# Optimization experiments

Hardware: AMD Instinct MI355X
Metric: run time of the kernel (lower is better)

The kernel has to match this reference:

```python
import jax, jax.numpy as jnp
import numpy as np

N = 100000          # nodes
DEG = 16            # fixed in-degree -> E = N*DEG edges
E = N * DEG
NEG_SLOPE = 0.2
HEADS = 4
HID = 64            # per-head hidden dim; layer width = HEADS*HID = 256
IN_DIM = 256
NUM_CLASSES = 41


def setup_inputs() -> dict:
    key = jax.random.key(0)
    ks = jax.random.split(key, 12)
    # CSC-style structure: for destination node i, col_ind[row_ptr[i]:row_ptr[i+1]] are its source neighbors
    row_ptr = (jnp.arange(N + 1, dtype=jnp.int32) * DEG)
    col_ind = jax.random.randint(ks[0], (E,), 0, N, dtype=jnp.int32)
    inputs = jax.random.normal(ks[1], (N, IN_DIM), dtype=jnp.float32)

    def glorot(k, shape):
        fan = sum(shape)
        return jax.random.normal(k, shape, dtype=jnp.float32) * jnp.sqrt(2.0 / fan)

    W0 = glorot(ks[2], (IN_DIM, HEADS * HID))
    al0 = glorot(ks[3], (HEADS, HID)); ar0 = glorot(ks[4], (HEADS, HID))
    W1 = glorot(ks[5], (HEADS * HID, HEADS * HID))
    al1 = glorot(ks[6], (HEADS, HID)); ar1 = glorot(ks[7], (HEADS, HID))
    W2 = glorot(ks[8], (HEADS * HID, HEADS * NUM_CLASSES))
    al2 = glorot(ks[9], (HEADS, NUM_CLASSES)); ar2 = glorot(ks[10], (HEADS, NUM_CLASSES))
    return {"row_ptr": row_ptr, "col_ind": col_ind, "inputs": inputs,
            "W0": W0, "al0": al0, "ar0": ar0,
            "W1": W1, "al1": al1, "ar1": ar1,
            "W2": W2, "al2": al2, "ar2": ar2}


def _gat_conv(h, W, a_l, a_r, src, dst, out_dim):
    # h: [N, F_in] -> feat: [N, H, D]
    feat = (h @ W).reshape(N, HEADS, out_dim)
    el = jnp.einsum('nhd,hd->nh', feat, a_l)   # [N, H] source-side score
    er = jnp.einsum('nhd,hd->nh', feat, a_r)   # [N, H] dest-side score
    e = jax.nn.leaky_relu(el[src] + er[dst], NEG_SLOPE)  # [E, H]
    # edge softmax over incoming edges of each destination node
    emax = jax.ops.segment_max(e, dst, num_segments=N)
    ex = jnp.exp(e - emax[dst])
    denom = jax.ops.segment_sum(ex, dst, num_segments=N)
    alpha = ex / denom[dst]                     # [E, H]
    # attention-weighted aggregation of source features
    msg = alpha[:, :, None] * feat[src]         # [E, H, D]
    return jax.ops.segment_sum(msg, dst, num_segments=N)  # [N, H, D]


def reference(row_ptr, col_ind, inputs, W0, al0, ar0, W1, al1, ar1, W2, al2, ar2):
    deg = jnp.diff(row_ptr)
    dst = jnp.repeat(jnp.arange(N, dtype=jnp.int32), deg, total_repeat_length=E)
    src = col_ind
    h = _gat_conv(inputs, W0, al0, ar0, src, dst, HID).reshape(N, HEADS * HID)
    h = _gat_conv(h, W1, al1, ar1, src, dst, HID).reshape(N, HEADS * HID)
    logits = _gat_conv(h, W2, al2, ar2, src, dst, NUM_CLASSES).mean(axis=1)  # [N, C]
    return logits
```

## Files before the change

### kernel.cpp

```cpp
#include <hip/hip_runtime.h>

#define NN 100000
#define DEG 16
#define HEADS 4
#define NEG_SLOPE 0.2f
#define NPAD 100096

typedef unsigned short ushort_t;
typedef __attribute__((ext_vector_type(8))) short bf16x8;
typedef __attribute__((ext_vector_type(4))) float f32x4;

__device__ __forceinline__ ushort_t f2bf_rn(float f) {
    uint32_t u = __float_as_uint(f);
    uint32_t r = (u + 0x7fffu + ((u >> 16) & 1u)) >> 16;
    return (ushort_t)r;
}
__device__ __forceinline__ float bf2f(ushort_t u) {
    return __uint_as_float(((uint32_t)u) << 16);
}

__global__ __launch_bounds__(256) void prep_wt(
    const float* __restrict__ W, ushort_t* __restrict__ Wh,
    ushort_t* __restrict__ Wl, int ncr)
{
    int idx = blockIdx.x * 256 + threadIdx.x;
    int n = idx >> 8, k = idx & 255;
    float v = (n < ncr) ? W[k * ncr + n] : 0.f;
    uint32_t b  = __float_as_uint(v);
    uint32_t hb = b & 0xffff0000u;
    float r = v - __uint_as_float(hb);
    Wh[idx] = (ushort_t)(hb >> 16);
    Wl[idx] = (ushort_t)(__float_as_uint(r) >> 16);
}

template <int AMODE, bool DO_SCORES>
__global__ __launch_bounds__(256) void gemm_mfma(
    const float* __restrict__ A32,
    const ushort_t* __restrict__ Ahi, const ushort_t* __restrict__ Alo,
    const ushort_t* __restrict__ Bth, const ushort_t* __restrict__ Btl,
    const float* __restrict__ al, const float* __restrict__ ar,
    ushort_t* __restrict__ Cb, int ldc, int ncr,
    float* __restrict__ el, float* __restrict__ er)
{
    __shared__ uint4 smem[2048];

    const int tid  = threadIdx.x;
    const int wv   = tid >> 6;
    const int ln   = tid & 63;
    const int wm   = wv >> 1;
    const int wn   = wv & 1;
    const int cl   = ln & 15;
    const int kq   = ln >> 4;
    const int row0 = blockIdx.y * 128;
    const int col0 = blockIdx.x * 128;

    f32x4 acc[4][4] = {};

    for (int k0 = 0; k0 < 256; k0 += 64) {
        if (k0) __syncthreads();
        if (AMODE == 1) {
            #pragma unroll
            for (int p = 0; p < 4; ++p) {
                int s = p * 256 + tid;
                int row = s >> 3, c = s & 7;
                int csw = c ^ (row & 7);
                size_t g = (size_t)(row0 + row) * 256 + k0 + c * 8;
                smem[row * 8 + csw]        = *reinterpret_cast<const uint4*>(Ahi + g);
                smem[1024 + row * 8 + csw] = *reinterpret_cast<const uint4*>(Alo + g);
            }
        } else {
            #pragma unroll
            for (int p = 0; p < 4; ++p) {
                int s = p * 256 + tid;
                int row = s >> 3, c = s & 7;
                int csw = c ^ (row & 7);
                int gr = row0 + row;
                float4 v0 = make_float4(0.f,0.f,0.f,0.f), v1 = v0;
                if (gr < NN) {
                    const float* g = A32 + (size_t)gr * 256 + k0 + c * 8;
                    v0 = *reinterpret_cast<const float4*>(g);
                    v1 = *reinterpret_cast<const float4*>(g + 4);
                }
                uint32_t b0 = __float_as_uint(v0.x), b1 = __float_as_uint(v0.y);
                uint32_t b2 = __float_as_uint(v0.z), b3 = __float_as_uint(v0.w);
                uint32_t b4 = __float_as_uint(v1.x), b5 = __float_as_uint(v1.y);
                uint32_t b6 = __float_as_uint(v1.z), b7 = __float_as_uint(v1.w);
                uint4 vh;
                vh.x = (b1 & 0xffff0000u) | (b0 >> 16);
                vh.y = (b3 & 0xffff0000u) | (b2 >> 16);
                vh.z = (b5 & 0xffff0000u) | (b4 >> 16);
                vh.w = (b7 & 0xffff0000u) | (b6 >> 16);
                float r0 = v0.x - __uint_as_float(b0 & 0xffff0000u);
                float r1 = v0.y - __uint_as_float(b1 & 0xffff0000u);
                float r2 = v0.z - __uint_as_float(b2 & 0xffff0000u);
                float r3 = v0.w - __uint_as_float(b3 & 0xffff0000u);
                float r4 = v1.x - __uint_as_float(b4 & 0xffff0000u);
                float r5 = v1.y - __uint_as_float(b5 & 0xffff0000u);
                float r6 = v1.z - __uint_as_float(b6 & 0xffff0000u);
                float r7 = v1.w - __uint_as_float(b7 & 0xffff0000u);
                uint4 vl;
                vl.x = (__float_as_uint(r1) & 0xffff0000u) | (__float_as_uint(r0) >> 16);
                vl.y = (__float_as_uint(r3) & 0xffff0000u) | (__float_as_uint(r2) >> 16);
                vl.z = (__float_as_uint(r5) & 0xffff0000u) | (__float_as_uint(r4) >> 16);
                vl.w = (__float_as_uint(r7) & 0xffff0000u) | (__float_as_uint(r6) >> 16);
                smem[row * 8 + csw]        = vh;
                smem[1024 + row * 8 + csw] = vl;
            }
        }
        __syncthreads();

        #pragma unroll
        for (int ksub = 0; ksub < 2; ++ksub) {
            bf16x8 ah[4], ax[4];
            #pragma unroll
            for (int mf = 0; mf < 4; ++mf) {
                int row = wm * 64 + mf * 16 + cl;
                int chunk = (ksub * 4 + kq) ^ (row & 7);
                int idx = row * 8 + chunk;
                ah[mf] = ((const bf16x8*)smem)[idx];
                ax[mf] = ((const bf16x8*)smem)[1024 + idx];
            }
            #pragma unroll
            for (int nf = 0; nf < 4; ++nf) {
                int colg = col0 + wn * 64 + nf * 16 + cl;
                size_t boff = (size_t)colg * 256 + k0 + ksub * 32 + kq * 8;
                bf16x8 bh = *reinterpret_cast<const bf16x8*>(Bth + boff);
                bf16x8 bl = *reinterpret_cast<const bf16x8*>(Btl + boff);
                #pragma unroll
                for (int mf = 0; mf < 4; ++mf) {
                    acc[mf][nf] = __builtin_amdgcn_mfma_f32_16x16x32_bf16(ah[mf], bh, acc[mf][nf], 0, 0, 0);
                    acc[mf][nf] = __builtin_amdgcn_mfma_f32_16x16x32_bf16(ah[mf], bl, acc[mf][nf], 0, 0, 0);
                    acc[mf][nf] = __builtin_amdgcn_mfma_f32_16x16x32_bf16(ax[mf], bh, acc[mf][nf], 0, 0, 0);
                }
            }
        }
    }

    #pragma unroll
    for (int mf = 0; mf < 4; ++mf) {
        int gr0 = row0 + wm * 64 + mf * 16 + kq * 4;
        #pragma unroll
        for (int r = 0; r < 4; ++r) {
            int gr = gr0 + r;
            if (gr < NN) {
                #pragma unroll
                for (int nf = 0; nf < 4; ++nf) {
                    int gc = col0 + wn * 64 + nf * 16 + cl;
                    if (gc < ncr)
                        Cb[(size_t)gr * ldc + gc] = f2bf_rn(acc[mf][nf][r]);
                }
            }
        }
    }

    if (DO_SCORES) {
        const int head = blockIdx.x * 2 + wn;
        float alv[4], arv[4];
        #pragma unroll
        for (int nf = 0; nf < 4; ++nf) {
            int d = nf * 16 + cl;
            alv[nf] = al[head * 64 + d];
            arv[nf] = ar[head * 64 + d];
        }
        #pragma unroll
        for (int mf = 0; mf < 4; ++mf) {
            #pragma unroll
            for (int r = 0; r < 4; ++r) {
                float pl = 0.f, pr = 0.f;
                #pragma unroll
                for (int nf = 0; nf < 4; ++nf) {
                    pl += acc[mf][nf][r] * alv[nf];
                    pr += acc[mf][nf][r] * arv[nf];
                }
                #pragma unroll
                for (int msk = 1; msk <= 8; msk <<= 1) {
                    pl += __shfl_xor(pl, msk);
                    pr += __shfl_xor(pr, msk);
                }
                if (cl == 0) {
                    int gr = row0 + wm * 64 + mf * 16 + kq * 4 + r;
                    if (gr < NN) {
                        el[gr * HEADS + head] = pl;
                        er[gr * HEADS + head] = pr;
                    }
                }
            }
        }
    }
}

__global__ __launch_bounds__(256) void scores2_bf(
    const ushort_t* __restrict__ featb, const float* __restrict__ al,
    const float* __restrict__ ar, float* __restrict__ el, float* __restrict__ er)
{
    const int n = blockIdx.x;
    const int t = threadIdx.x;
    const int h = t >> 6;
    const int j = t & 63;
    float v = 0.f, u = 0.f;
    if (j < 41) {
        float f = bf2f(featb[(size_t)n * 164 + h * 41 + j]);
        v = f * al[h * 41 + j];
        u = f * ar[h * 41 + j];
    }
    #pragma unroll
    for (int off = 32; off > 0; off >>= 1) {
        v += __shfl_down(v, off);
        u += __shfl_down(u, off);
    }
    if (j == 0) {
        el[n * HEADS + h] = v;
        er[n * HEADS + h] = u;
    }
}

__global__ __launch_bounds__(256) void agg_full_bf(
    const ushort_t* __restrict__ featb, const float* __restrict__ el,
    const float* __restrict__ er, const int* __restrict__ col,
    ushort_t* __restrict__ Hhi, ushort_t* __restrict__ Hlo)
{
    __shared__ int   s_src[4][DEG];
    __shared__ float s_alpha[4][HEADS][DEG];

    const int t = threadIdx.x;
    const int w = t >> 6;
    const int l = t & 63;
    const int n = blockIdx.x * 4 + w;
    const int h = l >> 4;
    const int k = l & 15;

    const int src_k = col[n * DEG + k];
    float x = el[src_k * HEADS + h] + er[n * HEADS + h];
    x = x > 0.f ? x : NEG_SLOPE * x;

    float m = x;
    #pragma unroll
    for (int msk = 8; msk >= 1; msk >>= 1) m = fmaxf(m, __shfl_xor(m, msk));
    float ex = __expf(x - m);
    float s = ex;
    #pragma unroll
    for (int msk = 8; msk >= 1; msk >>= 1) s += __shfl_xor(s, msk);

    s_alpha[w][h][k] = ex / s;
    if (l < DEG) s_src[w][l] = src_k;
    __syncthreads();

    float4 acc = make_float4(0.f, 0.f, 0.f, 0.f);
    #pragma unroll
    for (int k2 = 0; k2 < DEG; ++k2) {
        const int   sk = s_src[w][k2];
        const float a  = s_alpha[w][h][k2];
        ushort4 f = *reinterpret_cast<const ushort4*>(&featb[(size_t)sk * 256 + l * 4]);
        acc.x += a * bf2f(f.x);
        acc.y += a * bf2f(f.y);
        acc.z += a * bf2f(f.z);
        acc.w += a * bf2f(f.w);
    }
    uint32_t bx = __float_as_uint(acc.x), by = __float_as_uint(acc.y);
    uint32_t bz = __float_as_uint(acc.z), bw = __float_as_uint(acc.w);
    ushort4 hv;
    hv.x = (ushort_t)(bx >> 16); hv.y = (ushort_t)(by >> 16);
    hv.z = (ushort_t)(bz >> 16); hv.w = (ushort_t)(bw >> 16);
    float rx = acc.x - __uint_as_float(bx & 0xffff0000u);
    float ry = acc.y - __uint_as_float(by & 0xffff0000u);
    float rz = acc.z - __uint_as_float(bz & 0xffff0000u);
    float rw = acc.w - __uint_as_float(bw & 0xffff0000u);
    ushort4 lv;
    lv.x = (ushort_t)(__float_as_uint(rx) >> 16);
    lv.y = (ushort_t)(__float_as_uint(ry) >> 16);
    lv.z = (ushort_t)(__float_as_uint(rz) >> 16);
    lv.w = (ushort_t)(__float_as_uint(rw) >> 16);
    *reinterpret_cast<ushort4*>(&Hhi[(size_t)n * 256 + l * 4]) = hv;
    *reinterpret_cast<ushort4*>(&Hlo[(size_t)n * 256 + l * 4]) = lv;
}

__global__ __launch_bounds__(256) void agg_out_bf(
    const ushort_t* __restrict__ featb, const float* __restrict__ el,
    const float* __restrict__ er, const int* __restrict__ col,
    float* __restrict__ out)
{
    __shared__ int   s_src[4][DEG];
    __shared__ float s_alpha[4][HEADS][DEG];
    __shared__ float s_agg[4][164];

    const int t = threadIdx.x;
    const int w = t >> 6;
    const int l = t & 63;
    const int n = blockIdx.x * 4 + w;
    const int h = l >> 4;
    const int k = l & 15;

    const int src_k = col[n * DEG + k];
    float x = el[src_k * HEADS + h] + er[n * HEADS + h];
    x = x > 0.f ? x : NEG_SLOPE * x;

    float m = x;
    #pragma unroll
    for (int msk = 8; msk >= 1; msk >>= 1) m = fmaxf(m, __shfl_xor(m, msk));
    float ex = __expf(x - m);
    float s = ex;
    #pragma unroll
    for (int msk = 8; msk >= 1; msk >>= 1) s += __shfl_xor(s, msk);

    s_alpha[w][h][k] = ex / s;
    if (l < DEG) s_src[w][l] = src_k;
    __syncthreads();

    const int l41 = l < 41 ? l : 40;
    const int c0 = 4 * l41;
    const int h0 = (c0 + 0) / 41, h1 = (c0 + 1) / 41;
    const int h2 = (c0 + 2) / 41, h3 = (c0 + 3) / 41;

    float4 acc = make_float4(0.f, 0.f, 0.f, 0.f);
    #pragma unroll
    for (int k2 = 0; k2 < DEG; ++k2) {
        const int sk = s_src[w][k2];
        ushort4 f = *reinterpret_cast<const ushort4*>(&featb[(size_t)sk * 164 + c0]);
        acc.x += s_alpha[w][h0][k2] * bf2f(f.x);
        acc.y += s_alpha[w][h1][k2] * bf2f(f.y);
        acc.z += s_alpha[w][h2][k2] * bf2f(f.z);
        acc.w += s_alpha[w][h3][k2] * bf2f(f.w);
    }
    if (l < 41) *reinterpret_cast<float4*>(&s_agg[w][c0]) = acc;
    __syncthreads();
    if (l < 41)
        out[(size_t)n * 41 + l] =
            0.25f * (s_agg[w][l] + s_agg[w][l + 41] + s_agg[w][l + 82] + s_agg[w][l + 123]);
}

extern "C" void kernel_launch(void* const* d_in, const int* in_sizes, int n_in,
                              void* d_out, int out_size, void* d_ws, size_t ws_size,
                              hipStream_t stream)
{
    const int*   col_ind = (const int*)  d_in[1];
    const float* inputs  = (const float*)d_in[2];
    const float* W0      = (const float*)d_in[3];
    const float* al0     = (const float*)d_in[4];
    const float* ar0     = (const float*)d_in[5];
    const float* W1      = (const float*)d_in[6];
    const float* al1     = (const float*)d_in[7];
    const float* ar1     = (const float*)d_in[8];
    const float* W2      = (const float*)d_in[9];
    const float* al2     = (const float*)d_in[10];
    const float* ar2     = (const float*)d_in[11];
    float* out = (float*)d_out;

    char* ws = (char*)d_ws;
    const size_t seg = (size_t)NPAD * 256 * sizeof(ushort_t);
    ushort_t* h_hi  = (ushort_t*)(ws);
    ushort_t* h_lo  = (ushort_t*)(ws + seg);
    ushort_t* featb = (ushort_t*)(ws + 2 * seg);
    float*    el    = (float*)(ws + 3 * seg);
    float*    er    = el + (size_t)NN * HEADS;
    ushort_t* wt    = (ushort_t*)(er + (size_t)NN * HEADS);
    ushort_t* wt0h = wt;              ushort_t* wt0l = wt + 65536;
    ushort_t* wt1h = wt + 2 * 65536;  ushort_t* wt1l = wt + 3 * 65536;
    ushort_t* wt2h = wt + 4 * 65536;  ushort_t* wt2l = wt + 5 * 65536;

    dim3 blk(256);
    dim3 gg(2, (NN + 127) / 128);
    const int waveGrid = NN / 4;

    prep_wt<<<256, blk, 0, stream>>>(W0, wt0h, wt0l, 256);
    prep_wt<<<256, blk, 0, stream>>>(W1, wt1h, wt1l, 256);
    prep_wt<<<256, blk, 0, stream>>>(W2, wt2h, wt2l, 164);

    gemm_mfma<0, true><<<gg, blk, 0, stream>>>(
        inputs, nullptr, nullptr, wt0h, wt0l, al0, ar0, featb, 256, 256, el, er);
    agg_full_bf<<<waveGrid, blk, 0, stream>>>(featb, el, er, col_ind, h_hi, h_lo);

    gemm_mfma<1, true><<<gg, blk, 0, stream>>>(
        nullptr, h_hi, h_lo, wt1h, wt1l, al1, ar1, featb, 256, 256, el, er);
    agg_full_bf<<<waveGrid, blk, 0, stream>>>(featb, el, er, col_ind, h_hi, h_lo);

    gemm_mfma<1, false><<<gg, blk, 0, stream>>>(
        nullptr, h_hi, h_lo, wt2h, wt2l, nullptr, nullptr, featb, 164, 164, nullptr, nullptr);
    scores2_bf<<<NN, blk, 0, stream>>>(featb, al2, ar2, el, er);
    agg_out_bf<<<waveGrid, blk, 0, stream>>>(featb, el, er, col_ind, out);
}
```

Baseline: 752.2 us.

## Pre-swizzle weight tiles and stage B operand through shared memory

The weight-prep kernel now writes the bf16 hi/lo weight matrices in a fragment-ordered layout matching the MFMA lane mapping per 128-column block and 64-wide k-slice. The GEMM loads each k-slice of B into a new shared-memory buffer with coalesced 16-byte loads, then reads per-lane fragments from LDS instead of doing strided global loads inside the inner loop. This targets uncoalesced, repeated global B reads, at the cost of doubling shared memory per block, which may reduce occupancy.

```diff
diff --git a/kernel.cpp b/kernel.cpp
--- a/kernel.cpp
+++ b/kernel.cpp
@@ -24,8 +24,17 @@
     ushort_t* __restrict__ Wl, int ncr)
 {
     int idx = blockIdx.x * 256 + threadIdx.x;
-    int n = idx >> 8, k = idx & 255;
-    float v = (n < ncr) ? W[k * ncr + n] : 0.f;
+    int j     = idx & 7;
+    int chunk = idx >> 3;
+    int ln   = chunk & 63;
+    int nf   = (chunk >> 6) & 3;
+    int ksub = (chunk >> 8) & 1;
+    int wn   = (chunk >> 9) & 1;
+    int k0g  = (chunk >> 10) & 3;
+    int p    = (chunk >> 12) & 1;
+    int col = p * 128 + wn * 64 + nf * 16 + (ln & 15);
+    int k   = k0g * 64 + ksub * 32 + (ln >> 4) * 8 + j;
+    float v = (col < ncr) ? W[k * ncr + col] : 0.f;
     uint32_t b  = __float_as_uint(v);
     uint32_t hb = b & 0xffff0000u;
     float r = v - __uint_as_float(hb);
@@ -43,6 +52,7 @@
     float* __restrict__ el, float* __restrict__ er)
 {
     __shared__ uint4 smem[2048];
+    __shared__ uint4 smemB[2048];
 
     const int tid  = threadIdx.x;
     const int wv   = tid >> 6;
@@ -54,10 +64,26 @@
     const int row0 = blockIdx.y * 128;
     const int col0 = blockIdx.x * 128;
 
+    const ushort_t* bH = Bth + (size_t)blockIdx.x * 4 * 8192;
+    const ushort_t* bL = Btl + (size_t)blockIdx.x * 4 * 8192;
+
     f32x4 acc[4][4] = {};
 
-    for (int k0 = 0; k0 < 256; k0 += 64) {
+    for (int k0g = 0; k0g < 4; ++k0g) {
+        const int k0 = k0g * 64;
         if (k0) __syncthreads();
+
+        {
+            const ushort_t* rh = bH + k0g * 8192;
+            const ushort_t* rl = bL + k0g * 8192;
+            #pragma unroll
+            for (int q = 0; q < 4; ++q) {
+                int idx = q * 256 + tid;
+                smemB[idx]        = *reinterpret_cast<const uint4*>(rh + idx * 8);
+                smemB[1024 + idx] = *reinterpret_cast<const uint4*>(rl + idx * 8);
+            }
+        }
+
         if (AMODE == 1) {
             #pragma unroll
             for (int p = 0; p < 4; ++p) {
@@ -122,10 +148,9 @@
             }
             #pragma unroll
             for (int nf = 0; nf < 4; ++nf) {
-                int colg = col0 + wn * 64 + nf * 16 + cl;
-                size_t boff = (size_t)colg * 256 + k0 + ksub * 32 + kq * 8;
-                bf16x8 bh = *reinterpret_cast<const bf16x8*>(Bth + boff);
-                bf16x8 bl = *reinterpret_cast<const bf16x8*>(Btl + boff);
+                int bidx = ((wn * 2 + ksub) * 4 + nf) * 64 + ln;
+                bf16x8 bh = ((const bf16x8*)smemB)[bidx];
+                bf16x8 bl = ((const bf16x8*)smemB)[1024 + bidx];
                 #pragma unroll
                 for (int mf = 0; mf < 4; ++mf) {
                     acc[mf][nf] = __builtin_amdgcn_mfma_f32_16x16x32_bf16(ah[mf], bh, acc[mf][nf], 0, 0, 0);
```

New measurement: 658.1 us. -12.5%, faster.

## Double-buffer GEMM K-loop with direct global-to-LDS loads and pre-swizzled weights

Applied to the files above, without the earlier changes.

Rewrites the MFMA GEMM main loop into an 8-step, 32-wide K pipeline with two LDS buffers, so the next tile is prefetched while the current one is computed. A and B tiles are copied straight from global memory into LDS with global_load_lds, and the fp32-input path keeps its register prefetch and writes the converted tile after compute. The weight prep kernel now stores B already in MFMA fragment order, so each wave reads B from LDS instead of issuing scattered global loads. This doubles LDS use per block, which can lower occupancy, and the direct-to-LDS addressing depends on exact lane-to-address mapping.

```diff
diff --git a/kernel.cpp b/kernel.cpp
--- a/kernel.cpp
+++ b/kernel.cpp
@@ -19,13 +19,27 @@
     return __uint_as_float(((uint32_t)u) << 16);
 }
 
+__device__ __forceinline__ void gld16(const void* g, void* l) {
+    __builtin_amdgcn_global_load_lds(
+        (const __attribute__((address_space(1))) unsigned int*)g,
+        (__attribute__((address_space(3))) unsigned int*)l, 16, 0, 0);
+}
+
 __global__ __launch_bounds__(256) void prep_wt(
     const float* __restrict__ W, ushort_t* __restrict__ Wh,
     ushort_t* __restrict__ Wl, int ncr)
 {
     int idx = blockIdx.x * 256 + threadIdx.x;
-    int n = idx >> 8, k = idx & 255;
-    float v = (n < ncr) ? W[k * ncr + n] : 0.f;
+    int j     = idx & 7;
+    int chunk = idx >> 3;
+    int ln  = chunk & 63;
+    int nf  = (chunk >> 6) & 3;
+    int wn  = (chunk >> 8) & 1;
+    int k32 = (chunk >> 9) & 7;
+    int p   = (chunk >> 12) & 1;
+    int col = p * 128 + wn * 64 + nf * 16 + (ln & 15);
+    int k   = k32 * 32 + (ln >> 4) * 8 + j;
+    float v = (col < ncr) ? W[k * ncr + col] : 0.f;
     uint32_t b  = __float_as_uint(v);
     uint32_t hb = b & 0xffff0000u;
     float r = v - __uint_as_float(hb);
@@ -42,7 +56,7 @@
     ushort_t* __restrict__ Cb, int ldc, int ncr,
     float* __restrict__ el, float* __restrict__ er)
 {
-    __shared__ uint4 smem[2048];
+    __shared__ uint4 smem[4096];
 
     const int tid  = threadIdx.x;
     const int wv   = tid >> 6;
@@ -54,86 +68,135 @@
     const int row0 = blockIdx.y * 128;
     const int col0 = blockIdx.x * 128;
 
+    const ushort_t* bH = Bth + (size_t)blockIdx.x * 32768;
+    const ushort_t* bL = Btl + (size_t)blockIdx.x * 32768;
+
     f32x4 acc[4][4] = {};
-
-    for (int k0 = 0; k0 < 256; k0 += 64) {
-        if (k0) __syncthreads();
-        if (AMODE == 1) {
-            #pragma unroll
-            for (int p = 0; p < 4; ++p) {
-                int s = p * 256 + tid;
-                int row = s >> 3, c = s & 7;
-                int csw = c ^ (row & 7);
-                size_t g = (size_t)(row0 + row) * 256 + k0 + c * 8;
-                smem[row * 8 + csw]        = *reinterpret_cast<const uint4*>(Ahi + g);
-                smem[1024 + row * 8 + csw] = *reinterpret_cast<const uint4*>(Alo + g);
+    float4 ra0[2], ra1[2];
+
+    auto stageB = [&](int b, int step) {
+        const ushort_t* rh = bH + step * 4096;
+        const ushort_t* rl = bL + step * 4096;
+        char* dh = (char*)smem + b * 32768 + 16384;
+        char* dl = dh + 8192;
+        #pragma unroll
+        for (int q = 0; q < 2; ++q) {
+            int i = wv * 2 + q;
+            gld16(rh + (size_t)(i * 64 + ln) * 8, dh + i * 1024);
+            gld16(rl + (size_t)(i * 64 + ln) * 8, dl + i * 1024);
+        }
+    };
+    auto stageA1 = [&](int b, int step) {
+        const int rsub = ln >> 2;
+        const int c    = (ln & 3) ^ ((ln >> 3) & 3);
+        char* dh = (char*)smem + b * 32768;
+        char* dl = dh + 8192;
+        #pragma unroll
+        for (int q = 0; q < 2; ++q) {
+            int rb = wv * 2 + q;
+            size_t g = (size_t)(row0 + rb * 16 + rsub) * 256 + step * 32 + c * 8;
+            gld16(Ahi + g, dh + rb * 1024);
+            gld16(Alo + g, dl + rb * 1024);
+        }
+    };
+    auto loadA0 = [&](int step) {
+        #pragma unroll
+        for (int u = 0; u < 2; ++u) {
+            int qq = u * 256 + tid;
+            int row = qq >> 2, s = qq & 3;
+            int c = s ^ ((row >> 1) & 3);
+            int gr = row0 + row;
+            float4 v0 = make_float4(0.f, 0.f, 0.f, 0.f), v1 = v0;
+            if (gr < NN) {
+                const float* g = A32 + (size_t)gr * 256 + step * 32 + c * 8;
+                v0 = *reinterpret_cast<const float4*>(g);
+                v1 = *reinterpret_cast<const float4*>(g + 4);
             }
-        } else {
-            #pragma unroll
-            for (int p = 0; p < 4; ++p) {
-                int s = p * 256 + tid;
-                int row = s >> 3, c = s & 7;
-                int csw = c ^ (row & 7);
-                int gr = row0 + row;
-                float4 v0 = make_float4(0.f,0.f,0.f,0.f), v1 = v0;
-                if (gr < NN) {
-                    const float* g = A32 + (size_t)gr * 256 + k0 + c * 8;
-                    v0 = *reinterpret_cast<const float4*>(g);
-                    v1 = *reinterpret_cast<const float4*>(g + 4);
-                }
-                uint32_t b0 = __float_as_uint(v0.x), b1 = __float_as_uint(v0.y);
-                uint32_t b2 = __float_as_uint(v0.z), b3 = __float_as_uint(v0.w);
-                uint32_t b4 = __float_as_uint(v1.x), b5 = __float_as_uint(v1.y);
-                uint32_t b6 = __float_as_uint(v1.z), b7 = __float_as_uint(v1.w);
-                uint4 vh;
-                vh.x = (b1 & 0xffff0000u) | (b0 >> 16);
-                vh.y = (b3 & 0xffff0000u) | (b2 >> 16);
-                vh.z = (b5 & 0xffff0000u) | (b4 >> 16);
-                vh.w = (b7 & 0xffff0000u) | (b6 >> 16);
-                float r0 = v0.x - __uint_as_float(b0 & 0xffff0000u);
-                float r1 = v0.y - __uint_as_float(b1 & 0xffff0000u);
-                float r2 = v0.z - __uint_as_float(b2 & 0xffff0000u);
-                float r3 = v0.w - __uint_as_float(b3 & 0xffff0000u);
-                float r4 = v1.x - __uint_as_float(b4 & 0xffff0000u);
-                float r5 = v1.y - __uint_as_float(b5 & 0xffff0000u);
-                float r6 = v1.z - __uint_as_float(b6 & 0xffff0000u);
-                float r7 = v1.w - __uint_as_float(b7 & 0xffff0000u);
-                uint4 vl;
-                vl.x = (__float_as_uint(r1) & 0xffff0000u) | (__float_as_uint(r0) >> 16);
-                vl.y = (__float_as_uint(r3) & 0xffff0000u) | (__float_as_uint(r2) >> 16);
-                vl.z = (__float_as_uint(r5) & 0xffff0000u) | (__float_as_uint(r4) >> 16);
-                vl.w = (__float_as_uint(r7) & 0xffff0000u) | (__float_as_uint(r6) >> 16);
-                smem[row * 8 + csw]        = vh;
-                smem[1024 + row * 8 + csw] = vl;
-            }
-        }
-        __syncthreads();
-
-        #pragma unroll
-        for (int ksub = 0; ksub < 2; ++ksub) {
-            bf16x8 ah[4], ax[4];
+            ra0[u] = v0; ra1[u] = v1;
+        }
+    };
+    auto writeA0 = [&](int b) {
+        uint4* dh = smem + b * 2048;
+        uint4* dl = dh + 512;
+        #pragma unroll
+        for (int u = 0; u < 2; ++u) {
+            int qq = u * 256 + tid;
+            int row = qq >> 2, s = qq & 3;
+            float4 v0 = ra0[u], v1 = ra1[u];
+            uint32_t b0 = __float_as_uint(v0.x), b1 = __float_as_uint(v0.y);
+            uint32_t b2 = __float_as_uint(v0.z), b3 = __float_as_uint(v0.w);
+            uint32_t b4 = __float_as_uint(v1.x), b5 = __float_as_uint(v1.y);
+            uint32_t b6 = __float_as_uint(v1.z), b7 = __float_as_uint(v1.w);
+            uint4 vh;
+            vh.x = (b1 & 0xffff0000u) | (b0 >> 16);
+            vh.y = (b3 & 0xffff0000u) | (b2 >> 16);
+            vh.z = (b5 & 0xffff0000u) | (b4 >> 16);
+            vh.w = (b7 & 0xffff0000u) | (b6 >> 16);
+            float r0 = v0.x - __uint_as_float(b0 & 0xffff0000u);
+            float r1 = v0.y - __uint_as_float(b1 & 0xffff0000u);
+            float r2 = v0.z - __uint_as_float(b2 & 0xffff0000u);
+            float r3 = v0.w - __uint_as_float(b3 & 0xffff0000u);
+            float r4 = v1.x - __uint_as_float(b4 & 0xffff0000u);
+            float r5 = v1.y - __uint_as_float(b5 & 0xffff0000u);
+            float r6 = v1.z - __uint_as_float(b6 & 0xffff0000u);
+            float r7 = v1.w - __uint_as_float(b7 & 0xffff0000u);
+            uint4 vl;
+            vl.x = (__float_as_uint(r1) & 0xffff0000u) | (__float_as_uint(r0) >> 16);
+            vl.y = (__float_as_uint(r3) & 0xffff0000u) | (__float_as_uint(r2) >> 16);
+            vl.z = (__float_as_uint(r5) & 0xffff0000u) | (__float_as_uint(r4) >> 16);
+            vl.w = (__float_as_uint(r7) & 0xffff0000u) | (__float_as_uint(r6) >> 16);
+            dh[row * 4 + s] = vh;
+            dl[row * 4 + s] = vl;
+        }
+    };
+    auto compute = [&](int b) {
+        const bf16x8* aH  = (const bf16x8*)((char*)smem + b * 32768);
+        const bf16x8* aL  = (const bf16x8*)((char*)smem + b * 32768 + 8192);
+        const bf16x8* pbH = (const bf16x8*)((char*)smem + b * 32768 + 16384);
+        const bf16x8* pbL = (const bf16x8*)((char*)smem + b * 32768 + 24576);
+        bf16x8 ah[4], ax[4];
+        const int slot = kq ^ ((cl >> 1) & 3);
+        #pragma unroll
+        for (int mf = 0; mf < 4; ++mf) {
+            int row = wm * 64 + mf * 16 + cl;
+            int idx = row * 4 + slot;
+            ah[mf] = aH[idx];
+            ax[mf] = aL[idx];
+        }
+        #pragma unroll
+        for (int nf = 0; nf < 4; ++nf) {
+            int bidx = (wn * 4 + nf) * 64 + ln;
+            bf16x8 bh = pbH[bidx];
+            bf16x8 bl = pbL[bidx];
             #pragma unroll
             for (int mf = 0; mf < 4; ++mf) {
-                int row = wm * 64 + mf * 16 + cl;
-                int chunk = (ksub * 4 + kq) ^ (row & 7);
-                int idx = row * 8 + chunk;
-                ah[mf] = ((const bf16x8*)smem)[idx];
-                ax[mf] = ((const bf16x8*)smem)[1024 + idx];
+                acc[mf][nf] = __builtin_amdgcn_mfma_f32_16x16x32_bf16(ah[mf], bh, acc[mf][nf], 0, 0, 0);
+                acc[mf][nf] = __builtin_amdgcn_mfma_f32_16x16x32_bf16(ah[mf], bl, acc[mf][nf], 0, 0, 0);
+                acc[mf][nf] = __builtin_amdgcn_mfma_f32_16x16x32_bf16(ax[mf], bh, acc[mf][nf], 0, 0, 0);
             }
-            #pragma unroll
-            for (int nf = 0; nf < 4; ++nf) {
-                int colg = col0 + wn * 64 + nf * 16 + cl;
-                size_t boff = (size_t)colg * 256 + k0 + ksub * 32 + kq * 8;
-                bf16x8 bh = *reinterpret_cast<const bf16x8*>(Bth + boff);
-                bf16x8 bl = *reinterpret_cast<const bf16x8*>(Btl + boff);
-                #pragma unroll
-                for (int mf = 0; mf < 4; ++mf) {
-                    acc[mf][nf] = __builtin_amdgcn_mfma_f32_16x16x32_bf16(ah[mf], bh, acc[mf][nf], 0, 0, 0);
-                    acc[mf][nf] = __builtin_amdgcn_mfma_f32_16x16x32_bf16(ah[mf], bl, acc[mf][nf], 0, 0, 0);
-                    acc[mf][nf] = __builtin_amdgcn_mfma_f32_16x16x32_bf16(ax[mf], bh, acc[mf][nf], 0, 0, 0);
-                }
-            }
-        }
+        }
+    };
+
+    stageB(0, 0);
+    if (AMODE == 1) {
+        stageA1(0, 0);
+    } else {
+        loadA0(0);
+        writeA0(0);
+    }
+    __syncthreads();
+
+    #pragma unroll 2
+    for (int step = 0; step < 8; ++step) {
+        const int b = step & 1;
+        if (step < 7) {
+            stageB(b ^ 1, step + 1);
+            if (AMODE == 1) stageA1(b ^ 1, step + 1);
+            else            loadA0(step + 1);
+        }
+        compute(b);
+        if (AMODE == 0 && step < 7) writeA0(b ^ 1);
+        __syncthreads();
     }
 
     #pragma unroll
```

Measured after the change: 653.7 us. 13.1% less time.
